# Optimization experiments

Hardware: AMD Instinct MI355X
Metric: run time of the kernel (lower is better)

Reference implementation:

```python
import jax, jax.numpy as jnp
import numpy as np

B, S, DM, DC, L, NS = 4, 2048, 2048, 512, 4, 5  # batch, seq, d_model, d_cortical, n_layers, n_settle


def _ln(x, g, b):
    # torch nn.LayerNorm, eps=1e-5
    m = x.mean(-1, keepdims=True)
    v = ((x - m) ** 2).mean(-1, keepdims=True)
    return (x - m) * jax.lax.rsqrt(v + 1e-5) * g + b


def setup_inputs() -> dict:
    key = jax.random.key(0)
    ks = jax.random.split(key, 20)
    f = lambda k, sh: jax.random.normal(k, sh, jnp.float32) * 0.02
    return dict(
        qwen_final_hidden=jax.random.normal(ks[0], (B, S, DM), jnp.float32),
        obs=jax.random.normal(ks[1], (4, B, S, DM), jnp.float32),
        proj_W=f(ks[2], (4, DC, DM)), proj_b=f(ks[3], (4, DC)),
        fuse_W=f(ks[4], (DC, 4 * DC)), fuse_b=f(ks[5], (DC,)),
        up_W=f(ks[6], (L, DC, DC)), up_b=f(ks[7], (L, DC)),
        lateral_W=f(ks[8], (L, DC, DC)), lateral_b=f(ks[9], (L, DC)),
        precision_logit=f(ks[10], (L, DC)),
        ln_g=jnp.ones((L, DC), jnp.float32), ln_b=jnp.zeros((L, DC), jnp.float32),
        down_W=f(ks[11], (L - 1, DC, DC)), down_b=f(ks[12], (L - 1, DC)),
        out1_W=f(ks[13], (DC, DC)), out1_b=f(ks[14], (DC,)),
        out2_W=f(ks[15], (DM, DC)), out2_b=f(ks[16], (DM,)),
    )


def reference(qwen_final_hidden, obs, proj_W, proj_b, fuse_W, fuse_b,
              up_W, up_b, lateral_W, lateral_b, precision_logit,
              ln_g, ln_b, down_W, down_b, out1_W, out1_b, out2_W, out2_b):
    b, s, dm = qwen_final_hidden.shape
    # per-observed-layer input projections, concatenated along features
    proj = jnp.einsum('obsd,ocd->bsoc', obs, proj_W) + proj_b  # (B,S,4,DC)
    cat = proj.reshape(b, s, -1)
    fused = cat @ fuse_W.T + fuse_b                             # (B,S,DC)
    x0 = fused.reshape(b * s, DC)                               # per-token cortical input

    prec = jax.nn.sigmoid(precision_logit)                      # (L,DC)

    # initial bottom-up pass: activations = compress(x)
    acts = []
    x = x0
    for i in range(L):
        x = _ln(x @ up_W[i].T + up_b[i], ln_g[i], ln_b[i])
        acts.append(x)

    # settling iterations
    for _ in range(NS):
        # top-down predictions computed from pre-sweep activations
        preds = [None] * L
        for i in range(L - 1, 0, -1):
            if i < L - 1:  # top layer has no top-down weights
                preds[i - 1] = acts[i] @ down_W[i].T + down_b[i]
        x = x0
        for i in range(L):
            compressed = _ln(x @ up_W[i].T + up_b[i], ln_g[i], ln_b[i])
            target = preds[i] if preds[i] is not None else acts[i]
            werr = (compressed - target) * prec[i]
            lateral = acts[i] @ lateral_W[i].T + lateral_b[i]
            acts[i] = _ln(acts[i] + 0.5 * werr + 0.1 * lateral, ln_g[i], ln_b[i])
            x = acts[i]

    top = acts[-1]
    h = jax.nn.gelu(top @ out1_W.T + out1_b, approximate=False)
    correction = (h @ out2_W.T + out2_b).reshape(b, s, dm)
    return qwen_final_hidden + correction
```

## Files before the change

kernel.cpp:

```cpp
#include <hip/hip_runtime.h>
#include <hip/hip_bf16.h>
#include <math.h>

#define NTOK 8192
#define DMD  2048
#define DCC  512
#define TOKH 4194304

typedef __attribute__((ext_vector_type(8))) short short8;
typedef __attribute__((ext_vector_type(4))) float f32x4;

__device__ inline float bf2f(unsigned short u) {
    union { unsigned int i; float f; } x; x.i = ((unsigned int)u) << 16; return x.f;
}
__device__ inline unsigned short f2bf(float f) {
    union { float f; unsigned int i; } x; x.f = f;
    unsigned int u = x.i;
    return (unsigned short)((u + 0x7fffu + ((u >> 16) & 1u)) >> 16);
}

typedef const __attribute__((address_space(1))) unsigned int* gas1_t;
typedef __attribute__((address_space(3))) unsigned int* las3_t;
__device__ inline void async16(const void* g, void* l) {
    __builtin_amdgcn_global_load_lds(
        (gas1_t)g,
        (las3_t)(unsigned int)(unsigned long long)l, 16, 0, 0);
}

__device__ inline float wave_reduce_sum(float v) {
    #pragma unroll
    for (int off = 32; off > 0; off >>= 1) v += __shfl_xor(v, off, 64);
    return v;
}

__global__ __launch_bounds__(256)
void cvt_kernel(const float* __restrict__ s, unsigned short* __restrict__ d, int n4)
{
    int i = blockIdx.x * 256 + threadIdx.x;
    if (i >= n4) return;
    float4 v = ((const float4*)s)[i];
    ushort4 o;
    o.x = f2bf(v.x); o.y = f2bf(v.y); o.z = f2bf(v.z); o.w = f2bf(v.w);
    ((ushort4*)d)[i] = o;
}

struct GArgs {
    const unsigned short* A[6];
    const unsigned short* W[6];
    const float*          bias[6];
    const float*          add[6];
    void*                 C[6];
};

template<bool OUTF32, bool GELU>
__global__ __launch_bounds__(256)
void gemm16(GArgs ga, int lda, int ldw, int ldadd, int ldc, int K)
{
    __shared__ unsigned short As[128 * 32];
    __shared__ unsigned short Bs[128 * 32];

    const int z    = blockIdx.z;
    const int tid  = threadIdx.x;
    const int wave = tid >> 6;
    const int lane = tid & 63;
    const int bm   = blockIdx.y * 128;
    const int bn   = blockIdx.x * 128;
    const int wr   = wave >> 1;
    const int wc   = wave & 1;

    const unsigned short* Ap = ga.A[z];
    const unsigned short* Wp = ga.W[z];

    const int lrow = lane >> 2;
    const int lcol = (lane & 3) * 8;

    f32x4 acc[4][4] = {};

    for (int k0 = 0; k0 < K; k0 += 32) {
        #pragma unroll
        for (int r = 0; r < 2; ++r) {
            int c = wave + r * 4;
            async16(Ap + (size_t)(bm + c * 16 + lrow) * lda + k0 + lcol, As + c * 512);
            async16(Wp + (size_t)(bn + c * 16 + lrow) * ldw + k0 + lcol, Bs + c * 512);
        }
        __syncthreads();

        short8 af[4], bfr[4];
        #pragma unroll
        for (int i = 0; i < 4; ++i) {
            af[i]  = *(const short8*)&As[(wr * 64 + i * 16 + (lane & 15)) * 32 + (lane >> 4) * 8];
            bfr[i] = *(const short8*)&Bs[(wc * 64 + i * 16 + (lane & 15)) * 32 + (lane >> 4) * 8];
        }
        #pragma unroll
        for (int mi = 0; mi < 4; ++mi)
            #pragma unroll
            for (int ni = 0; ni < 4; ++ni)
                acc[mi][ni] = __builtin_amdgcn_mfma_f32_16x16x32_bf16(
                    af[mi], bfr[ni], acc[mi][ni], 0, 0, 0);
        __syncthreads();
    }

    const float* bias = ga.bias[z];
    const float* add  = ga.add[z];
    #pragma unroll
    for (int ni = 0; ni < 4; ++ni) {
        int col = bn + wc * 64 + ni * 16 + (lane & 15);
        float bv = bias ? bias[col] : 0.0f;
        #pragma unroll
        for (int mi = 0; mi < 4; ++mi) {
            #pragma unroll
            for (int r = 0; r < 4; ++r) {
                int row = bm + wr * 64 + mi * 16 + (lane >> 4) * 4 + r;
                float vv = acc[mi][ni][r] + bv;
                if (GELU) vv = 0.5f * vv * (1.0f + erff(vv * 0.7071067811865475f));
                if (OUTF32) {
                    if (add) vv += add[(size_t)row * ldadd + col];
                    ((float*)ga.C[z])[(size_t)row * ldc + col] = vv;
                } else {
                    ((unsigned short*)ga.C[z])[(size_t)row * ldc + col] = f2bf(vv);
                }
            }
        }
    }
}

__global__ __launch_bounds__(256)
void ln16_kernel(const unsigned short* __restrict__ src, const float* __restrict__ g,
                 const float* __restrict__ b, unsigned short* __restrict__ dst)
{
    const int token = blockIdx.x * 4 + (threadIdx.x >> 6);
    const int lane  = threadIdx.x & 63;
    const size_t base = (size_t)token * DCC + lane * 8;
    const int c0 = lane * 8;

    short8 raw = *(const short8*)(src + base);
    float x[8], s = 0.f, q = 0.f;
    #pragma unroll
    for (int j = 0; j < 8; ++j) {
        x[j] = bf2f((unsigned short)raw[j]);
        s += x[j]; q += x[j] * x[j];
    }
    s = wave_reduce_sum(s); q = wave_reduce_sum(q);
    float m = s * (1.0f / DCC);
    float r = rsqrtf(q * (1.0f / DCC) - m * m + 1e-5f);

    float4 g0 = *(const float4*)(g + c0), g1 = *(const float4*)(g + c0 + 4);
    float4 b0 = *(const float4*)(b + c0), b1 = *(const float4*)(b + c0 + 4);
    float gg[8] = {g0.x,g0.y,g0.z,g0.w,g1.x,g1.y,g1.z,g1.w};
    float bb[8] = {b0.x,b0.y,b0.z,b0.w,b1.x,b1.y,b1.z,b1.w};

    short8 o;
    #pragma unroll
    for (int j = 0; j < 8; ++j)
        o[j] = (short)f2bf((x[j] - m) * r * gg[j] + bb[j]);
    *(short8*)(dst + base) = o;
}

__global__ __launch_bounds__(256)
void update16_kernel(const unsigned short* __restrict__ z,
                     const unsigned short* a,
                     const unsigned short* t,
                     const unsigned short* __restrict__ lat,
                     const float* __restrict__ logit,
                     const float* __restrict__ g,
                     const float* __restrict__ b,
                     unsigned short* outp)
{
    const int token = blockIdx.x * 4 + (threadIdx.x >> 6);
    const int lane  = threadIdx.x & 63;
    const size_t base = (size_t)token * DCC + lane * 8;
    const int c0 = lane * 8;

    short8 zr = *(const short8*)(z + base);
    float zv[8], s = 0.f, q = 0.f;
    #pragma unroll
    for (int j = 0; j < 8; ++j) {
        zv[j] = bf2f((unsigned short)zr[j]);
        s += zv[j]; q += zv[j] * zv[j];
    }
    s = wave_reduce_sum(s); q = wave_reduce_sum(q);
    float m1 = s * (1.0f / DCC);
    float r1 = rsqrtf(q * (1.0f / DCC) - m1 * m1 + 1e-5f);

    float4 g0 = *(const float4*)(g + c0), g1 = *(const float4*)(g + c0 + 4);
    float4 b0 = *(const float4*)(b + c0), b1 = *(const float4*)(b + c0 + 4);
    float4 p0 = *(const float4*)(logit + c0), p1 = *(const float4*)(logit + c0 + 4);
    float gg[8] = {g0.x,g0.y,g0.z,g0.w,g1.x,g1.y,g1.z,g1.w};
    float bb[8] = {b0.x,b0.y,b0.z,b0.w,b1.x,b1.y,b1.z,b1.w};
    float pv[8] = {p0.x,p0.y,p0.z,p0.w,p1.x,p1.y,p1.z,p1.w};

    short8 ar = *(const short8*)(a + base);
    short8 tr = *(const short8*)(t + base);
    short8 lr = *(const short8*)(lat + base);

    float tv[8], s2 = 0.f, q2 = 0.f;
    #pragma unroll
    for (int j = 0; j < 8; ++j) {
        float comp = (zv[j] - m1) * r1 * gg[j] + bb[j];
        float prec = 1.0f / (1.0f + __expf(-pv[j]));
        float val  = bf2f((unsigned short)ar[j])
                   + 0.5f * (comp - bf2f((unsigned short)tr[j])) * prec
                   + 0.1f * bf2f((unsigned short)lr[j]);
        tv[j] = val;
        s2 += val; q2 += val * val;
    }
    s2 = wave_reduce_sum(s2); q2 = wave_reduce_sum(q2);
    float m2 = s2 * (1.0f / DCC);
    float r2 = rsqrtf(q2 * (1.0f / DCC) - m2 * m2 + 1e-5f);

    short8 o;
    #pragma unroll
    for (int j = 0; j < 8; ++j)
        o[j] = (short)f2bf((tv[j] - m2) * r2 * gg[j] + bb[j]);
    *(short8*)(outp + base) = o;
}

extern "C" void kernel_launch(void* const* d_in, const int* in_sizes, int n_in,
                              void* d_out, int out_size, void* d_ws, size_t ws_size,
                              hipStream_t stream)
{
    const float* qwen   = (const float*)d_in[0];
    const float* obs    = (const float*)d_in[1];
    const float* proj_W = (const float*)d_in[2];
    const float* proj_b = (const float*)d_in[3];
    const float* fuse_W = (const float*)d_in[4];
    const float* fuse_b = (const float*)d_in[5];
    const float* up_W   = (const float*)d_in[6];
    const float* up_b   = (const float*)d_in[7];
    const float* lat_W  = (const float*)d_in[8];
    const float* lat_b  = (const float*)d_in[9];
    const float* plogit = (const float*)d_in[10];
    const float* ln_g   = (const float*)d_in[11];
    const float* ln_b   = (const float*)d_in[12];
    const float* down_W = (const float*)d_in[13];
    const float* down_b = (const float*)d_in[14];
    const float* out1_W = (const float*)d_in[15];
    const float* out1_b = (const float*)d_in[16];
    const float* out2_W = (const float*)d_in[17];
    const float* out2_b = (const float*)d_in[18];
    float* out = (float*)d_out;

    unsigned short* wsu = (unsigned short*)d_ws;
    unsigned short* catbuf = wsu;
    unsigned short* x0b    = wsu + 16777216;
    unsigned short* acts16[4] = {
        wsu + 20971520, wsu + 20971520 + TOKH,
        wsu + 20971520 + 2 * TOKH, wsu + 20971520 + 3 * TOKH };
    unsigned short* w16    = wsu + 37748736;
    unsigned short* projW16 = w16;
    unsigned short* fuseW16 = w16 + 4194304;
    unsigned short* upW16   = w16 + 5242880;
    unsigned short* latW16  = w16 + 6291456;
    unsigned short* downW16 = w16 + 7340032;
    unsigned short* out1W16 = w16 + 8126464;
    unsigned short* out2W16 = w16 + 8388608;
    unsigned short* h16     = catbuf;

    unsigned short* outu = (unsigned short*)d_out;
    unsigned short* pred16a = outu;
    unsigned short* pred16b = outu + TOKH;
    unsigned short* z16     = outu + 2 * TOKH;
    unsigned short* lat16[4] = { outu + 3*TOKH, outu + 4*TOKH, outu + 5*TOKH, outu + 6*TOKH };

    dim3 blk(256);
    dim3 lngrid(NTOK / 4);

    auto cvt = [&](const float* s, unsigned short* d, int n) {
        int n4 = n / 4;
        cvt_kernel<<<dim3((n4 + 255) / 256), blk, 0, stream>>>(s, d, n4);
    };
    cvt(proj_W, projW16, 4 * DCC * DMD);
    cvt(fuse_W, fuseW16, DCC * 4 * DCC);
    cvt(up_W,   upW16,   4 * DCC * DCC);
    cvt(lat_W,  latW16,  4 * DCC * DCC);
    cvt(down_W, downW16, 3 * DCC * DCC);
    cvt(out1_W, out1W16, DCC * DCC);
    cvt(out2_W, out2W16, DMD * DCC);

    for (int p = 0; p < 2; ++p) {
        cvt(obs + (size_t)p * 2 * NTOK * DMD, outu, 2 * NTOK * DMD);
        GArgs a{};
        for (int q = 0; q < 2; ++q) {
            int o = 2 * p + q;
            a.A[q]    = outu + (size_t)q * NTOK * DMD;
            a.W[q]    = projW16 + (size_t)o * DCC * DMD;
            a.bias[q] = proj_b + o * DCC;
            a.C[q]    = catbuf + o * DCC;
        }
        gemm16<false, false><<<dim3(DCC/128, NTOK/128, 2), blk, 0, stream>>>(
            a, DMD, DMD, 0, 4 * DCC, DMD);
    }
    {
        GArgs a{};
        a.A[0] = catbuf; a.W[0] = fuseW16; a.bias[0] = fuse_b; a.C[0] = x0b;
        gemm16<false, false><<<dim3(DCC/128, NTOK/128, 1), blk, 0, stream>>>(
            a, 4 * DCC, 4 * DCC, 0, DCC, 4 * DCC);
    }

    for (int i = 0; i < 4; ++i) {
        GArgs a{};
        a.A[0] = (i == 0) ? x0b : acts16[i - 1];
        a.W[0] = upW16 + (size_t)i * DCC * DCC;
        a.bias[0] = up_b + i * DCC;
        a.C[0] = z16;
        gemm16<false, false><<<dim3(DCC/128, NTOK/128, 1), blk, 0, stream>>>(
            a, DCC, DCC, 0, DCC, DCC);
        ln16_kernel<<<lngrid, blk, 0, stream>>>(z16, ln_g + i * DCC, ln_b + i * DCC, acts16[i]);
    }

    for (int s = 0; s < 5; ++s) {
        {
            GArgs a{};
            a.A[0] = acts16[1]; a.W[0] = downW16 + (size_t)1 * DCC * DCC;
            a.bias[0] = down_b + 1 * DCC; a.C[0] = pred16a;
            a.A[1] = acts16[2]; a.W[1] = downW16 + (size_t)2 * DCC * DCC;
            a.bias[1] = down_b + 2 * DCC; a.C[1] = pred16b;
            for (int i = 0; i < 4; ++i) {
                a.A[2 + i] = acts16[i];
                a.W[2 + i] = latW16 + (size_t)i * DCC * DCC;
                a.bias[2 + i] = lat_b + i * DCC;
                a.C[2 + i] = lat16[i];
            }
            gemm16<false, false><<<dim3(DCC/128, NTOK/128, 6), blk, 0, stream>>>(
                a, DCC, DCC, 0, DCC, DCC);
        }
        for (int i = 0; i < 4; ++i) {
            GArgs a{};
            a.A[0] = (i == 0) ? x0b : acts16[i - 1];
            a.W[0] = upW16 + (size_t)i * DCC * DCC;
            a.bias[0] = up_b + i * DCC;
            a.C[0] = z16;
            gemm16<false, false><<<dim3(DCC/128, NTOK/128, 1), blk, 0, stream>>>(
                a, DCC, DCC, 0, DCC, DCC);
            const unsigned short* tgt = (i == 0) ? pred16a : (i == 1) ? pred16b : acts16[i];
            update16_kernel<<<lngrid, blk, 0, stream>>>(
                z16, acts16[i], tgt, lat16[i],
                plogit + i * DCC, ln_g + i * DCC, ln_b + i * DCC, acts16[i]);
        }
    }

    {
        GArgs a{};
        a.A[0] = acts16[3]; a.W[0] = out1W16; a.bias[0] = out1_b; a.C[0] = h16;
        gemm16<false, true><<<dim3(DCC/128, NTOK/128, 1), blk, 0, stream>>>(
            a, DCC, DCC, 0, DCC, DCC);
    }
    {
        GArgs a{};
        a.A[0] = h16; a.W[0] = out2W16; a.bias[0] = out2_b;
        a.add[0] = qwen; a.C[0] = out;
        gemm16<true, false><<<dim3(DMD/128, NTOK/128, 1), blk, 0, stream>>>(
            a, DCC, DCC, DMD, DMD, DCC);
    }
}
```

Before: 1.653 ms.

## Fuse up-projection GEMM with LayerNorm/update and convert obs inside projection GEMM

Adds a full-row (32x512 tile) GEMM kernel that computes the up-projection and applies LayerNorm, plus the precision-weighted update and second LayerNorm, in its epilogue. This removes the z16 intermediate round trip and the separate ln/update kernel launches. The obs fp32→bf16 conversion now happens inside the projection GEMM's A-tile load, so a full bf16 copy of obs is no longer written and read. All weight conversions are merged into one launch. The trade-offs are synchronous fp32 A loads instead of async LDS loads in the projection GEMM, and fewer, larger blocks (256) in the fused kernel.

```diff
diff --git a/kernel.cpp b/kernel.cpp
--- a/kernel.cpp
+++ b/kernel.cpp
@@ -27,21 +27,26 @@
         (las3_t)(unsigned int)(unsigned long long)l, 16, 0, 0);
 }
 
-__device__ inline float wave_reduce_sum(float v) {
-    #pragma unroll
-    for (int off = 32; off > 0; off >>= 1) v += __shfl_xor(v, off, 64);
-    return v;
-}
+struct CvtArgs { const float* src[7]; };
 
 __global__ __launch_bounds__(256)
-void cvt_kernel(const float* __restrict__ s, unsigned short* __restrict__ d, int n4)
+void wcvt_kernel(CvtArgs ca, unsigned short* __restrict__ dst)
 {
-    int i = blockIdx.x * 256 + threadIdx.x;
-    if (i >= n4) return;
-    float4 v = ((const float4*)s)[i];
-    ushort4 o;
-    o.x = f2bf(v.x); o.y = f2bf(v.y); o.z = f2bf(v.z); o.w = f2bf(v.w);
-    ((ushort4*)d)[i] = o;
+    const int total = 2359296;
+    for (int i = blockIdx.x * 256 + threadIdx.x; i < total; i += gridDim.x * 256) {
+        const float* sp; int base;
+        if      (i < 1048576) { sp = ca.src[0]; base = 0;       }
+        else if (i < 1310720) { sp = ca.src[1]; base = 1048576; }
+        else if (i < 1572864) { sp = ca.src[2]; base = 1310720; }
+        else if (i < 1835008) { sp = ca.src[3]; base = 1572864; }
+        else if (i < 2031616) { sp = ca.src[4]; base = 1835008; }
+        else if (i < 2097152) { sp = ca.src[5]; base = 2031616; }
+        else                  { sp = ca.src[6]; base = 2097152; }
+        float4 v = ((const float4*)sp)[i - base];
+        ushort4 o;
+        o.x = f2bf(v.x); o.y = f2bf(v.y); o.z = f2bf(v.z); o.w = f2bf(v.w);
+        ((ushort4*)dst)[i] = o;
+    }
 }
 
 struct GArgs {
@@ -52,7 +57,7 @@
     void*                 C[6];
 };
 
-template<bool OUTF32, bool GELU>
+template<bool A32, bool OUTF32, bool GELU>
 __global__ __launch_bounds__(256)
 void gemm16(GArgs ga, int lda, int ldw, int ldadd, int ldc, int K)
 {
@@ -77,10 +82,27 @@
     f32x4 acc[4][4] = {};
 
     for (int k0 = 0; k0 < K; k0 += 32) {
+        if constexpr (A32) {
+            const float* Af = (const float*)Ap;
+            #pragma unroll
+            for (int r = 0; r < 4; ++r) {
+                int idx = r * 256 + tid;
+                int row = idx >> 3, c4 = (idx & 7) * 4;
+                float4 v = *(const float4*)(Af + (size_t)(bm + row) * lda + k0 + c4);
+                ushort4 o;
+                o.x = f2bf(v.x); o.y = f2bf(v.y); o.z = f2bf(v.z); o.w = f2bf(v.w);
+                *(ushort4*)&As[row * 32 + c4] = o;
+            }
+        } else {
+            #pragma unroll
+            for (int r = 0; r < 2; ++r) {
+                int c = wave + r * 4;
+                async16(Ap + (size_t)(bm + c * 16 + lrow) * lda + k0 + lcol, As + c * 512);
+            }
+        }
         #pragma unroll
         for (int r = 0; r < 2; ++r) {
             int c = wave + r * 4;
-            async16(Ap + (size_t)(bm + c * 16 + lrow) * lda + k0 + lcol, As + c * 512);
             async16(Wp + (size_t)(bn + c * 16 + lrow) * ldw + k0 + lcol, Bs + c * 512);
         }
         __syncthreads();
@@ -124,95 +146,179 @@
     }
 }
 
+__device__ inline int csw(int rl, int col) {
+    return rl * 512 + (col ^ (((rl >> 2) & 3) << 4));
+}
+
+template<int MODE>
 __global__ __launch_bounds__(256)
-void ln16_kernel(const unsigned short* __restrict__ src, const float* __restrict__ g,
-                 const float* __restrict__ b, unsigned short* __restrict__ dst)
+void gemm_fused(const unsigned short* __restrict__ Ap,
+                const unsigned short* __restrict__ Wp,
+                const float* __restrict__ bias,
+                const float* __restrict__ g,
+                const float* __restrict__ b,
+                const unsigned short* a_in,
+                const unsigned short* t_in,
+                const unsigned short* __restrict__ lat_in,
+                const float* __restrict__ logit,
+                unsigned short* outp)
 {
-    const int token = blockIdx.x * 4 + (threadIdx.x >> 6);
-    const int lane  = threadIdx.x & 63;
-    const size_t base = (size_t)token * DCC + lane * 8;
-    const int c0 = lane * 8;
-
-    short8 raw = *(const short8*)(src + base);
-    float x[8], s = 0.f, q = 0.f;
-    #pragma unroll
-    for (int j = 0; j < 8; ++j) {
-        x[j] = bf2f((unsigned short)raw[j]);
-        s += x[j]; q += x[j] * x[j];
-    }
-    s = wave_reduce_sum(s); q = wave_reduce_sum(q);
-    float m = s * (1.0f / DCC);
-    float r = rsqrtf(q * (1.0f / DCC) - m * m + 1e-5f);
-
-    float4 g0 = *(const float4*)(g + c0), g1 = *(const float4*)(g + c0 + 4);
-    float4 b0 = *(const float4*)(b + c0), b1 = *(const float4*)(b + c0 + 4);
-    float gg[8] = {g0.x,g0.y,g0.z,g0.w,g1.x,g1.y,g1.z,g1.w};
-    float bb[8] = {b0.x,b0.y,b0.z,b0.w,b1.x,b1.y,b1.z,b1.w};
-
-    short8 o;
-    #pragma unroll
-    for (int j = 0; j < 8; ++j)
-        o[j] = (short)f2bf((x[j] - m) * r * gg[j] + bb[j]);
-    *(short8*)(dst + base) = o;
-}
-
-__global__ __launch_bounds__(256)
-void update16_kernel(const unsigned short* __restrict__ z,
-                     const unsigned short* a,
-                     const unsigned short* t,
-                     const unsigned short* __restrict__ lat,
-                     const float* __restrict__ logit,
-                     const float* __restrict__ g,
-                     const float* __restrict__ b,
-                     unsigned short* outp)
-{
-    const int token = blockIdx.x * 4 + (threadIdx.x >> 6);
-    const int lane  = threadIdx.x & 63;
-    const size_t base = (size_t)token * DCC + lane * 8;
-    const int c0 = lane * 8;
-
-    short8 zr = *(const short8*)(z + base);
-    float zv[8], s = 0.f, q = 0.f;
-    #pragma unroll
-    for (int j = 0; j < 8; ++j) {
-        zv[j] = bf2f((unsigned short)zr[j]);
-        s += zv[j]; q += zv[j] * zv[j];
-    }
-    s = wave_reduce_sum(s); q = wave_reduce_sum(q);
-    float m1 = s * (1.0f / DCC);
-    float r1 = rsqrtf(q * (1.0f / DCC) - m1 * m1 + 1e-5f);
-
-    float4 g0 = *(const float4*)(g + c0), g1 = *(const float4*)(g + c0 + 4);
-    float4 b0 = *(const float4*)(b + c0), b1 = *(const float4*)(b + c0 + 4);
-    float4 p0 = *(const float4*)(logit + c0), p1 = *(const float4*)(logit + c0 + 4);
-    float gg[8] = {g0.x,g0.y,g0.z,g0.w,g1.x,g1.y,g1.z,g1.w};
-    float bb[8] = {b0.x,b0.y,b0.z,b0.w,b1.x,b1.y,b1.z,b1.w};
-    float pv[8] = {p0.x,p0.y,p0.z,p0.w,p1.x,p1.y,p1.z,p1.w};
-
-    short8 ar = *(const short8*)(a + base);
-    short8 tr = *(const short8*)(t + base);
-    short8 lr = *(const short8*)(lat + base);
-
-    float tv[8], s2 = 0.f, q2 = 0.f;
-    #pragma unroll
-    for (int j = 0; j < 8; ++j) {
-        float comp = (zv[j] - m1) * r1 * gg[j] + bb[j];
-        float prec = 1.0f / (1.0f + __expf(-pv[j]));
-        float val  = bf2f((unsigned short)ar[j])
-                   + 0.5f * (comp - bf2f((unsigned short)tr[j])) * prec
-                   + 0.1f * bf2f((unsigned short)lr[j]);
-        tv[j] = val;
-        s2 += val; q2 += val * val;
-    }
-    s2 = wave_reduce_sum(s2); q2 = wave_reduce_sum(q2);
-    float m2 = s2 * (1.0f / DCC);
-    float r2 = rsqrtf(q2 * (1.0f / DCC) - m2 * m2 + 1e-5f);
-
-    short8 o;
-    #pragma unroll
-    for (int j = 0; j < 8; ++j)
-        o[j] = (short)f2bf((tv[j] - m2) * r2 * gg[j] + bb[j]);
-    *(short8*)(outp + base) = o;
+    __shared__ unsigned short As[2][32 * 32];
+    __shared__ unsigned short Bs[2][512 * 32];
+    __shared__ float red[2][4][32];
+
+    const int tid  = threadIdx.x;
+    const int wave = tid >> 6;
+    const int lane = tid & 63;
+    const int lrow = lane >> 2;
+    const int lc8  = (lane & 3) * 8;
+    const int bm   = blockIdx.x * 32;
+    const int l15  = lane & 15;
+    const int lh   = lane >> 4;
+
+    f32x4 acc[2][8] = {};
+
+    if (wave < 2)
+        async16(Ap + (size_t)(bm + wave * 16 + lrow) * DCC + lc8, &As[0][wave * 512]);
+    #pragma unroll
+    for (int r = 0; r < 8; ++r)
+        async16(Wp + (size_t)((r * 4 + wave) * 16 + lrow) * DCC + lc8,
+                &Bs[0][(r * 4 + wave) * 512]);
+    __syncthreads();
+
+    for (int t = 0; t < 16; ++t) {
+        const int cur = t & 1;
+        if (t < 15) {
+            const int k0 = (t + 1) * 32;
+            if (wave < 2)
+                async16(Ap + (size_t)(bm + wave * 16 + lrow) * DCC + k0 + lc8,
+                        &As[cur ^ 1][wave * 512]);
+            #pragma unroll
+            for (int r = 0; r < 8; ++r)
+                async16(Wp + (size_t)((r * 4 + wave) * 16 + lrow) * DCC + k0 + lc8,
+                        &Bs[cur ^ 1][(r * 4 + wave) * 512]);
+        }
+        short8 af[2], bfr[8];
+        #pragma unroll
+        for (int mi = 0; mi < 2; ++mi)
+            af[mi] = *(const short8*)&As[cur][(mi * 16 + l15) * 32 + lh * 8];
+        #pragma unroll
+        for (int ni = 0; ni < 8; ++ni)
+            bfr[ni] = *(const short8*)&Bs[cur][(wave * 128 + ni * 16 + l15) * 32 + lh * 8];
+        #pragma unroll
+        for (int mi = 0; mi < 2; ++mi)
+            #pragma unroll
+            for (int ni = 0; ni < 8; ++ni)
+                acc[mi][ni] = __builtin_amdgcn_mfma_f32_16x16x32_bf16(
+                    af[mi], bfr[ni], acc[mi][ni], 0, 0, 0);
+        __syncthreads();
+    }
+
+    float bv[8], gv[8], bbv[8];
+    #pragma unroll
+    for (int ni = 0; ni < 8; ++ni) {
+        int col = wave * 128 + ni * 16 + l15;
+        bv[ni] = bias[col]; gv[ni] = g[col]; bbv[ni] = b[col];
+    }
+
+    float ps[2][4], pq[2][4];
+    #pragma unroll
+    for (int mi = 0; mi < 2; ++mi)
+        #pragma unroll
+        for (int rr = 0; rr < 4; ++rr) {
+            float s = 0.f, q = 0.f;
+            #pragma unroll
+            for (int ni = 0; ni < 8; ++ni) {
+                float v = acc[mi][ni][rr] + bv[ni];
+                acc[mi][ni][rr] = v;
+                s += v; q += v * v;
+            }
+            #pragma unroll
+            for (int off = 1; off < 16; off <<= 1) {
+                s += __shfl_xor(s, off, 64);
+                q += __shfl_xor(q, off, 64);
+            }
+            ps[mi][rr] = s; pq[mi][rr] = q;
+        }
+    if (l15 == 0) {
+        #pragma unroll
+        for (int mi = 0; mi < 2; ++mi)
+            #pragma unroll
+            for (int rr = 0; rr < 4; ++rr) {
+                int rl = mi * 16 + lh * 4 + rr;
+                red[0][wave][rl] = ps[mi][rr];
+                red[1][wave][rl] = pq[mi][rr];
+            }
+    }
+    __syncthreads();
+
+    unsigned short* compS = &Bs[0][0];
+    #pragma unroll
+    for (int mi = 0; mi < 2; ++mi)
+        #pragma unroll
+        for (int rr = 0; rr < 4; ++rr) {
+            int rl = mi * 16 + lh * 4 + rr;
+            float s = red[0][0][rl] + red[0][1][rl] + red[0][2][rl] + red[0][3][rl];
+            float q = red[1][0][rl] + red[1][1][rl] + red[1][2][rl] + red[1][3][rl];
+            float m1 = s * (1.0f / DCC);
+            float r1 = rsqrtf(q * (1.0f / DCC) - m1 * m1 + 1e-5f);
+            #pragma unroll
+            for (int ni = 0; ni < 8; ++ni) {
+                int col = wave * 128 + ni * 16 + l15;
+                compS[csw(rl, col)] = f2bf((acc[mi][ni][rr] - m1) * r1 * gv[ni] + bbv[ni]);
+            }
+        }
+    __syncthreads();
+
+    float gr[8], br[8], pr[8];
+    if constexpr (MODE == 1) {
+        const int c0 = lane * 8;
+        float4 g0 = *(const float4*)(g + c0),     g1 = *(const float4*)(g + c0 + 4);
+        float4 b0 = *(const float4*)(b + c0),     b1 = *(const float4*)(b + c0 + 4);
+        float4 p0 = *(const float4*)(logit + c0), p1 = *(const float4*)(logit + c0 + 4);
+        float gt[8] = {g0.x,g0.y,g0.z,g0.w,g1.x,g1.y,g1.z,g1.w};
+        float bt[8] = {b0.x,b0.y,b0.z,b0.w,b1.x,b1.y,b1.z,b1.w};
+        float pt[8] = {p0.x,p0.y,p0.z,p0.w,p1.x,p1.y,p1.z,p1.w};
+        #pragma unroll
+        for (int j = 0; j < 8; ++j) {
+            gr[j] = gt[j]; br[j] = bt[j];
+            pr[j] = 1.0f / (1.0f + __expf(-pt[j]));
+        }
+    }
+
+    #pragma unroll
+    for (int rr = 0; rr < 8; ++rr) {
+        const int rl = wave * 8 + rr;
+        const size_t gbase = (size_t)(bm + rl) * DCC + lane * 8;
+        short8 cm = *(const short8*)&compS[csw(rl, lane * 8)];
+        if constexpr (MODE == 0) {
+            *(short8*)(outp + gbase) = cm;
+        } else {
+            short8 ar = *(const short8*)(a_in + gbase);
+            short8 tr = *(const short8*)(t_in + gbase);
+            short8 lr = *(const short8*)(lat_in + gbase);
+            float tv[8], s = 0.f, q = 0.f;
+            #pragma unroll
+            for (int j = 0; j < 8; ++j) {
+                float val = bf2f((unsigned short)ar[j])
+                          + 0.5f * (bf2f((unsigned short)cm[j]) - bf2f((unsigned short)tr[j])) * pr[j]
+                          + 0.1f * bf2f((unsigned short)lr[j]);
+                tv[j] = val; s += val; q += val * val;
+            }
+            #pragma unroll
+            for (int off = 1; off < 64; off <<= 1) {
+                s += __shfl_xor(s, off, 64);
+                q += __shfl_xor(q, off, 64);
+            }
+            float m2 = s * (1.0f / DCC);
+            float r2 = rsqrtf(q * (1.0f / DCC) - m2 * m2 + 1e-5f);
+            short8 o;
+            #pragma unroll
+            for (int j = 0; j < 8; ++j)
+                o[j] = (short)f2bf((tv[j] - m2) * r2 * gr[j] + br[j]);
+            *(short8*)(outp + gbase) = o;
+        }
+    }
 }
 
 extern "C" void kernel_launch(void* const* d_in, const int* in_sizes, int n_in,
@@ -259,53 +365,42 @@
     unsigned short* outu = (unsigned short*)d_out;
     unsigned short* pred16a = outu;
     unsigned short* pred16b = outu + TOKH;
-    unsigned short* z16     = outu + 2 * TOKH;
-    unsigned short* lat16[4] = { outu + 3*TOKH, outu + 4*TOKH, outu + 5*TOKH, outu + 6*TOKH };
+    unsigned short* lat16[4] = { outu + 2*TOKH, outu + 3*TOKH, outu + 4*TOKH, outu + 5*TOKH };
 
     dim3 blk(256);
-    dim3 lngrid(NTOK / 4);
-
-    auto cvt = [&](const float* s, unsigned short* d, int n) {
-        int n4 = n / 4;
-        cvt_kernel<<<dim3((n4 + 255) / 256), blk, 0, stream>>>(s, d, n4);
-    };
-    cvt(proj_W, projW16, 4 * DCC * DMD);
-    cvt(fuse_W, fuseW16, DCC * 4 * DCC);
-    cvt(up_W,   upW16,   4 * DCC * DCC);
-    cvt(lat_W,  latW16,  4 * DCC * DCC);
-    cvt(down_W, downW16, 3 * DCC * DCC);
-    cvt(out1_W, out1W16, DCC * DCC);
-    cvt(out2_W, out2W16, DMD * DCC);
-
-    for (int p = 0; p < 2; ++p) {
-        cvt(obs + (size_t)p * 2 * NTOK * DMD, outu, 2 * NTOK * DMD);
+
+    {
+        CvtArgs ca;
+        ca.src[0] = proj_W; ca.src[1] = fuse_W; ca.src[2] = up_W;
+        ca.src[3] = lat_W;  ca.src[4] = down_W; ca.src[5] = out1_W;
+        ca.src[6] = out2_W;
+        wcvt_kernel<<<dim3(2048), blk, 0, stream>>>(ca, w16);
+    }
+
+    {
         GArgs a{};
-        for (int q = 0; q < 2; ++q) {
-            int o = 2 * p + q;
-            a.A[q]    = outu + (size_t)q * NTOK * DMD;
-            a.W[q]    = projW16 + (size_t)o * DCC * DMD;
-            a.bias[q] = proj_b + o * DCC;
-            a.C[q]    = catbuf + o * DCC;
-        }
-        gemm16<false, false><<<dim3(DCC/128, NTOK/128, 2), blk, 0, stream>>>(
+        for (int o = 0; o < 4; ++o) {
+            a.A[o]    = (const unsigned short*)(obs + (size_t)o * NTOK * DMD);
+            a.W[o]    = projW16 + (size_t)o * DCC * DMD;
+            a.bias[o] = proj_b + o * DCC;
+            a.C[o]    = catbuf + o * DCC;
+        }
+        gemm16<true, false, false><<<dim3(DCC/128, NTOK/128, 4), blk, 0, stream>>>(
             a, DMD, DMD, 0, 4 * DCC, DMD);
     }
     {
         GArgs a{};
         a.A[0] = catbuf; a.W[0] = fuseW16; a.bias[0] = fuse_b; a.C[0] = x0b;
-        gemm16<false, false><<<dim3(DCC/128, NTOK/128, 1), blk, 0, stream>>>(
+        gemm16<false, false, false><<<dim3(DCC/128, NTOK/128, 1), blk, 0, stream>>>(
             a, 4 * DCC, 4 * DCC, 0, DCC, 4 * DCC);
     }
 
     for (int i = 0; i < 4; ++i) {
-        GArgs a{};
-        a.A[0] = (i == 0) ? x0b : acts16[i - 1];
-        a.W[0] = upW16 + (size_t)i * DCC * DCC;
-        a.bias[0] = up_b + i * DCC;
-        a.C[0] = z16;
-        gemm16<false, false><<<dim3(DCC/128, NTOK/128, 1), blk, 0, stream>>>(
-            a, DCC, DCC, 0, DCC, DCC);
-        ln16_kernel<<<lngrid, blk, 0, stream>>>(z16, ln_g + i * DCC, ln_b + i * DCC, acts16[i]);
+        gemm_fused<0><<<dim3(NTOK/32), blk, 0, stream>>>(
+            (i == 0) ? x0b : acts16[i - 1],
+            upW16 + (size_t)i * DCC * DCC, up_b + i * DCC,
+            ln_g + i * DCC, ln_b + i * DCC,
+            nullptr, nullptr, nullptr, nullptr, acts16[i]);
     }
 
     for (int s = 0; s < 5; ++s) {
@@ -321,35 +416,31 @@
                 a.bias[2 + i] = lat_b + i * DCC;
                 a.C[2 + i] = lat16[i];
             }
-            gemm16<false, false><<<dim3(DCC/128, NTOK/128, 6), blk, 0, stream>>>(
+            gemm16<false, false, false><<<dim3(DCC/128, NTOK/128, 6), blk, 0, stream>>>(
                 a, DCC, DCC, 0, DCC, DCC);
         }
         for (int i = 0; i < 4; ++i) {
-            GArgs a{};
-            a.A[0] = (i == 0) ? x0b : acts16[i - 1];
-            a.W[0] = upW16 + (size_t)i * DCC * DCC;
-            a.bias[0] = up_b + i * DCC;
-            a.C[0] = z16;
-            gemm16<false, false><<<dim3(DCC/128, NTOK/128, 1), blk, 0, stream>>>(
-                a, DCC, DCC, 0, DCC, DCC);
-            const unsigned short* tgt = (i == 0) ? pred16a : (i == 1) ? pred16b : acts16[i];
-            update16_kernel<<<lngrid, blk, 0, stream>>>(
-                z16, acts16[i], tgt, lat16[i],
-                plogit + i * DCC, ln_g + i * DCC, ln_b + i * DCC, acts16[i]);
+            const unsigned short* tgt =
+                (i == 0) ? pred16a : (i == 1) ? pred16b : acts16[i];
+            gemm_fused<1><<<dim3(NTOK/32), blk, 0, stream>>>(
+                (i == 0) ? x0b : acts16[i - 1],
+                upW16 + (size_t)i * DCC * DCC, up_b + i * DCC,
+                ln_g + i * DCC, ln_b + i * DCC,
+                acts16[i], tgt, lat16[i], plogit + i * DCC, acts16[i]);
         }
     }
 
     {
         GArgs a{};
         a.A[0] = acts16[3]; a.W[0] = out1W16; a.bias[0] = out1_b; a.C[0] = h16;
-        gemm16<false, true><<<dim3(DCC/128, NTOK/128, 1), blk, 0, stream>>>(
+        gemm16<false, false, true><<<dim3(DCC/128, NTOK/128, 1), blk, 0, stream>>>(
             a, DCC, DCC, 0, DCC, DCC);
     }
     {
         GArgs a{};
         a.A[0] = h16; a.W[0] = out2W16; a.bias[0] = out2_b;
         a.add[0] = qwen; a.C[0] = out;
-        gemm16<true, false><<<dim3(DMD/128, NTOK/128, 1), blk, 0, stream>>>(
+        gemm16<false, true, false><<<dim3(DMD/128, NTOK/128, 1), blk, 0, stream>>>(
             a, DCC, DCC, DMD, DMD, DCC);
     }
 }
```

Result: no change. 1.683 ms (+1.8%).
